# Kernel tuning notes

Hardware: AMD Instinct MI355X
Metric: run time of the kernel (lower is better)

The kernel has to match this reference:

```python
import jax, jax.numpy as jnp
import numpy as np

N = 4096        # number_of_users
IN = 1000       # in_size (items)
H1, H2 = 2048, 1024
EMB = 512
HEADS = 8
OUT = 1000


def setup_inputs() -> dict:
    key = jax.random.key(0)
    ks = iter(jax.random.split(key, 32))
    def lin(i, o):
        return jax.random.normal(next(ks), (i, o), jnp.float32) * (1.0 / np.sqrt(i))
    inp = {"batch": jax.random.normal(next(ks), (N, IN), jnp.float32)}
    for p in ("q", "k", "v"):
        inp[p + "_w1"] = lin(IN, H1); inp[p + "_b1"] = jnp.zeros((H1,), jnp.float32)
        inp[p + "_w2"] = lin(H1, H2); inp[p + "_b2"] = jnp.zeros((H2,), jnp.float32)
        inp[p + "_w3"] = lin(H2, EMB); inp[p + "_b3"] = jnp.zeros((EMB,), jnp.float32)
    inp["wo_w"] = lin(EMB, OUT)
    inp["wo_b"] = jnp.zeros((OUT,), jnp.float32)
    return inp


def _mlp(x, w1, b1, w2, b2, w3, b3):
    h = jax.nn.relu(x @ w1 + b1)
    h = jax.nn.relu(h @ w2 + b2)
    return h @ w3 + b3


def _split_heads(x):
    # [N, EMB] -> [HEADS, N, depth]
    return x.reshape(N, HEADS, EMB // HEADS).transpose(1, 0, 2)


def reference(batch,
              q_w1, q_b1, q_w2, q_b2, q_w3, q_b3,
              k_w1, k_b1, k_w2, k_b2, k_w3, k_b3,
              v_w1, v_b1, v_w2, v_b2, v_w3, v_b3,
              wo_w, wo_b):
    q = _mlp(batch, q_w1, q_b1, q_w2, q_b2, q_w3, q_b3)
    k = _mlp(batch, k_w1, k_b1, k_w2, k_b2, k_w3, k_b3)
    v = _mlp(batch, v_w1, v_b1, v_w2, v_b2, v_w3, v_b3)
    qh = jax.nn.relu(_split_heads(q))
    kh = jax.nn.relu(_split_heads(k))
    vh = _split_heads(v)
    depth = EMB // HEADS
    # ReLU-normalized attention (no softmax): scores / row-sum
    scores = jnp.einsum('hnd,hmd->hnm', qh, kh) / jnp.sqrt(jnp.float32(depth))
    denom = jnp.sum(scores, axis=-1, keepdims=True) + 1e-8
    weights = scores / denom
    att = jnp.einsum('hnm,hmd->hnd', weights, vh)   # [H, N, depth]
    att = att.transpose(1, 0, 2).reshape(N, EMB)
    return att @ wo_w + wo_b
```

## Files before the change

### kernel.cpp

```cpp
#include <hip/hip_runtime.h>
#include <hip/hip_bf16.h>


typedef __attribute__((ext_vector_type(4))) float f32x4;
typedef __attribute__((ext_vector_type(4))) float float4v;
typedef __attribute__((ext_vector_type(8))) short bf16x8;

static constexpr size_t OFF_XB   = 0;
static constexpr size_t OFF_WT1  = OFF_XB   + 8388608;
static constexpr size_t OFF_WT2  = OFF_WT1  + 12582912;
static constexpr size_t OFF_WT3  = OFF_WT2  + 12582912;
static constexpr size_t OFF_MWT  = OFF_WT3  + 3145728;
static constexpr size_t OFF_B1C  = OFF_MWT  + 1048576;
static constexpr size_t OFF_H1   = OFF_B1C  + 24576;
static constexpr size_t OFF_H2   = OFF_H1   + 50331648;
static constexpr size_t OFF_QKV  = OFF_H2   + 25165824;
static constexpr size_t OFF_MP   = OFF_QKV  + 12582912;
static constexpr size_t OFF_MF   = OFF_MP   + 4259840;
static constexpr size_t OFF_QT   = OFF_MF   + 133120;

__device__ __forceinline__ void gload16(const __hip_bfloat16* g, __hip_bfloat16* l) {
  __builtin_amdgcn_global_load_lds(
      (const __attribute__((address_space(1))) void*)g,
      (__attribute__((address_space(3))) void*)l, 16, 0, 0);
}

__device__ __forceinline__ void xcd_map(int gx, int gy, int cm, int cn,
                                        int& zz, int& mt, int& nt) {
  const int gid = (blockIdx.z * gy + blockIdx.y) * gx + blockIdx.x;
  const int xcd = gid & 7;
  const int slot = gid >> 3;
  const int per = cm * cn;
  zz = slot / per;
  const int rem = slot % per;
  const int nxr = gx / cn;
  const int xr = xcd % nxr, yr = xcd / nxr;
  mt = yr * cm + rem % cm;
  nt = xr * cn + rem / cm;
}

__global__ __launch_bounds__(256) void prep(
    const float* __restrict__ w1a, const float* __restrict__ w1b, const float* __restrict__ w1c,
    const float* __restrict__ w2a, const float* __restrict__ w2b, const float* __restrict__ w2c,
    const float* __restrict__ w3a, const float* __restrict__ w3b, const float* __restrict__ w3c,
    const float* __restrict__ batch,
    __hip_bfloat16* __restrict__ WT1, __hip_bfloat16* __restrict__ WT2,
    __hip_bfloat16* __restrict__ WT3, __hip_bfloat16* __restrict__ XB) {
  __shared__ float tile[32][33];
  const int b = blockIdx.x, t = threadIdx.x;
  if (b >= 13824) {
    int idx = (b - 13824) * 256 + t;
    int row = idx >> 8, c4 = (idx & 255) * 4;
    __hip_bfloat16 o[4];
    if (c4 < 1000) {
      float4v v = *reinterpret_cast<const float4v*>(&batch[(size_t)row * 1000 + c4]);
#pragma unroll
      for (int j = 0; j < 4; ++j) o[j] = __float2bfloat16(v[j]);
    } else {
#pragma unroll
      for (int j = 0; j < 4; ++j) o[j] = __float2bfloat16(0.f);
    }
    *reinterpret_cast<ushort4*>(&XB[(size_t)row * 1024 + c4]) =
        *reinterpret_cast<const ushort4*>(o);
    return;
  }
  const float* in; __hip_bfloat16* out; int K, N, Kpad, kb, nb;
  if (b < 6144) {
    int mat = b >> 11, r = b & 2047;
    const float* s[3] = {w1a, w1b, w1c};
    in = s[mat]; out = WT1 + (size_t)mat * 2048 * 1024;
    K = 1000; N = 2048; Kpad = 1024; kb = r & 31; nb = r >> 5;
  } else if (b < 12288) {
    int r = b - 6144; int mat = r >> 11; r &= 2047;
    const float* s[3] = {w2a, w2b, w2c};
    in = s[mat]; out = WT2 + (size_t)mat * 1024 * 2048;
    K = 2048; N = 1024; Kpad = 2048; kb = r & 63; nb = r >> 6;
  } else {
    int r = b - 12288; int mat = r >> 9; r &= 511;
    const float* s[3] = {w3a, w3b, w3c};
    in = s[mat]; out = WT3 + (size_t)mat * 512 * 1024;
    K = 1024; N = 512; Kpad = 1024; kb = r & 31; nb = r >> 5;
  }
  const int tx = t & 31, ty = t >> 5;
  const int kb32 = kb * 32, nb32 = nb * 32;
  for (int i = ty; i < 32; i += 8) {
    int k = kb32 + i, n = nb32 + tx;
    tile[i][tx] = (k < K && n < N) ? in[(size_t)k * N + n] : 0.f;
  }
  __syncthreads();
  for (int i = ty; i < 32; i += 8) {
    int n = nb32 + i, kp = kb32 + tx;
    out[(size_t)n * Kpad + kp] = __float2bfloat16(tile[tx][i]);
  }
}

__global__ __launch_bounds__(256) void gemm_fast(
    const __hip_bfloat16* __restrict__ A, int lda, size_t Az,
    const __hip_bfloat16* __restrict__ B, int ldb, size_t Bz,
    const float* __restrict__ bias0, const float* __restrict__ bias1,
    const float* __restrict__ bias2,
    void* __restrict__ Cout, int ldc, size_t Cz,
    int nlimit, int NT, int epi, int cm, int cn) {
  __shared__ __hip_bfloat16 smA[2][4096];
  __shared__ __hip_bfloat16 smB[2][4096];
  const int t = threadIdx.x;
  int zz, mt, nt;
  xcd_map(gridDim.x, gridDim.y, cm, cn, zz, mt, nt);
  const int m0 = mt * 128, n0 = nt * 128;
  A += (size_t)zz * Az;
  B += (size_t)zz * Bz;

  const int w = t >> 6, l = t & 63;
  const int wm = (w >> 1) * 64, wn = (w & 1) * 64;
  const int fr = l & 15, fq = l >> 4;

  const int r0 = t >> 2;
  const int cg = (t & 3) ^ ((t >> 3) & 3);
  const __hip_bfloat16* gA0 = A + (size_t)(m0 + r0) * lda + cg * 8;
  const __hip_bfloat16* gA1 = gA0 + (size_t)64 * lda;
  const __hip_bfloat16* gB0 = B + (size_t)(n0 + r0) * ldb + cg * 8;
  const __hip_bfloat16* gB1 = gB0 + (size_t)64 * ldb;

  const int soff = (fq ^ ((fr >> 1) & 3)) * 8;
  int offA[4], offB[4];
#pragma unroll
  for (int i = 0; i < 4; ++i) {
    offA[i] = (wm + i * 16 + fr) * 32 + soff;
    offB[i] = (wn + i * 16 + fr) * 32 + soff;
  }

  f32x4 acc[4][4] = {};

  gload16(gA0, &smA[0][w * 512]);
  gload16(gA1, &smA[0][w * 512 + 2048]);
  gload16(gB0, &smB[0][w * 512]);
  gload16(gB1, &smB[0][w * 512 + 2048]);
  asm volatile("s_waitcnt vmcnt(0)" ::: "memory");
  __builtin_amdgcn_s_barrier();

  for (int T = 0; T < NT; ++T) {
    const int cur = T & 1, nxt = cur ^ 1;
    if (T > 0) {
      asm volatile("s_waitcnt vmcnt(0) lgkmcnt(0)" ::: "memory");
      __builtin_amdgcn_sched_barrier(0);
      __builtin_amdgcn_s_barrier();
    }
    bf16x8 af[4], bf[4];
#pragma unroll
    for (int i = 0; i < 4; ++i) {
      af[i] = *reinterpret_cast<const bf16x8*>(&smA[cur][offA[i]]);
      bf[i] = *reinterpret_cast<const bf16x8*>(&smB[cur][offB[i]]);
    }
    if (T + 1 < NT) {
      const size_t ko = (size_t)(T + 1) * 32;
      gload16(gA0 + ko, &smA[nxt][w * 512]);
      gload16(gA1 + ko, &smA[nxt][w * 512 + 2048]);
      gload16(gB0 + ko, &smB[nxt][w * 512]);
      gload16(gB1 + ko, &smB[nxt][w * 512 + 2048]);
    }
    __builtin_amdgcn_s_setprio(1);
#pragma unroll
    for (int i = 0; i < 4; ++i)
#pragma unroll
      for (int j = 0; j < 4; ++j)
        acc[i][j] = __builtin_amdgcn_mfma_f32_16x16x32_bf16(af[i], bf[j], acc[i][j], 0, 0, 0);
    __builtin_amdgcn_s_setprio(0);
  }

  const float* bz = (zz == 0) ? bias0 : ((zz == 1) ? bias1 : bias2);
  const bool dorelu = (epi == 1) || (epi == 4) || (epi == 3 && zz < 2);
  float bv[4];
#pragma unroll
  for (int j = 0; j < 4; ++j) {
    const int col = n0 + wn + j * 16 + fr;
    if (epi == 4) {
      const float* bsel = (col < 2048) ? bias0 : ((col < 4096) ? bias1 : bias2);
      bv[j] = bsel[col & 2047];
    } else if (epi == 2) {
      bv[j] = (col < nlimit) ? bias0[col] : 0.f;
    } else {
      bv[j] = bz[col];
    }
  }
#pragma unroll
  for (int i = 0; i < 4; ++i) {
#pragma unroll
    for (int j = 0; j < 4; ++j) {
      const int col = n0 + wn + j * 16 + fr;
#pragma unroll
      for (int rr = 0; rr < 4; ++rr) {
        const int row = m0 + wm + i * 16 + fq * 4 + rr;
        float v = acc[i][j][rr] + bv[j];
        if (dorelu) v = fmaxf(v, 0.f);
        if (epi == 2) {
          if (col < nlimit)
            ((float*)Cout)[(size_t)row * ldc + col] = v;
        } else {
          ((__hip_bfloat16*)Cout + (size_t)zz * Cz)[(size_t)row * ldc + col] =
              __float2bfloat16(v);
        }
      }
    }
  }
}

__global__ __launch_bounds__(256) void kv_outer(const __hip_bfloat16* __restrict__ QKV, int ld,
                                                float* __restrict__ part) {
  __shared__ __hip_bfloat16 kt[128][64];
  __shared__ __hip_bfloat16 vt[128][64];
  const int t = threadIdx.x;
  const int n0 = blockIdx.x * 128;
  const int h = blockIdx.y;
#pragma unroll
  for (int it = 0; it < 4; ++it) {
    int r = it * 32 + (t >> 3);
    int c = (t & 7) * 8;
    const __hip_bfloat16* kr = &QKV[(size_t)(n0 + r) * ld + 512 + h * 64 + c];
    const __hip_bfloat16* vr = &QKV[(size_t)(n0 + r) * ld + 1024 + h * 64 + c];
    *reinterpret_cast<bf16x8*>(&kt[r][c]) = *reinterpret_cast<const bf16x8*>(kr);
    *reinterpret_cast<bf16x8*>(&vt[r][c]) = *reinterpret_cast<const bf16x8*>(vr);
  }
  __syncthreads();
  const int i = t >> 2, j0 = (t & 3) << 4;
  float acc[16] = {};
  float ks = 0.f;
  for (int r = 0; r < 128; ++r) {
    float kv = __bfloat162float(kt[r][i]);
    ks += kv;
    bf16x8 va = *reinterpret_cast<const bf16x8*>(&vt[r][j0]);
    bf16x8 vb = *reinterpret_cast<const bf16x8*>(&vt[r][j0 + 8]);
#pragma unroll
    for (int jj = 0; jj < 8; ++jj) {
      ushort ua = (ushort)((const short*)&va)[jj];
      ushort ub = (ushort)((const short*)&vb)[jj];
      acc[jj]     += kv * __bfloat162float(*(const __hip_bfloat16*)&ua);
      acc[8 + jj] += kv * __bfloat162float(*(const __hip_bfloat16*)&ub);
    }
  }
  float* dst = part + ((size_t)blockIdx.x * 8 + h) * 4160;
#pragma unroll
  for (int jj = 0; jj < 16; ++jj) dst[i * 64 + j0 + jj] = acc[jj];
  if ((t & 3) == 0) dst[4096 + i] = ks;
}

__global__ void reduce_m(const float* __restrict__ part, float* __restrict__ Mfin) {
  int h = blockIdx.x, t = threadIdx.x;
  for (int idx = t; idx < 4160; idx += 256) {
    float s = 0.f;
    for (int c = 0; c < 32; ++c) s += part[((size_t)c * 8 + h) * 4160 + idx];
    Mfin[(size_t)h * 4160 + idx] = s;
  }
}

__global__ __launch_bounds__(256) void mwq(const float* __restrict__ Mfin,
                                           const float* __restrict__ wo,
                                           __hip_bfloat16* __restrict__ MWT,
                                           const __hip_bfloat16* __restrict__ QKV,
                                           __hip_bfloat16* __restrict__ QT) {
  const int t = threadIdx.x;
  if (blockIdx.x < 32) {
    __shared__ float Ml[64][64];
    const int h = blockIdx.x >> 2;
    const int j = (blockIdx.x & 3) * 256 + t;
    const float* M = Mfin + (size_t)h * 4160;
    for (int e = t; e < 4096; e += 256)
      Ml[e >> 6][e & 63] = M[e];
    __syncthreads();
    float wcol[64];
    const bool valid = (j < 1000);
#pragma unroll
    for (int d = 0; d < 64; ++d)
      wcol[d] = valid ? wo[(size_t)(h * 64 + d) * 1000 + j] : 0.f;
    short ob[64];
#pragma unroll
    for (int i = 0; i < 64; ++i) {
      float a = 0.f;
#pragma unroll
      for (int d = 0; d < 64; ++d) a += Ml[i][d] * wcol[d];
      __hip_bfloat16 bb = __float2bfloat16(a);
      ob[i] = *(const short*)&bb;
    }
    __hip_bfloat16* dst = MWT + (size_t)j * 512 + h * 64;
#pragma unroll
    for (int v = 0; v < 8; ++v)
      *reinterpret_cast<bf16x8*>(dst + v * 8) = *reinterpret_cast<const bf16x8*>(&ob[v * 8]);
  } else {
    const int bid = blockIdx.x - 32;
    const int r = bid * 4 + (t >> 6);
    const int c = (t & 63) * 8;
    const int h = (t & 63) >> 3;
    bf16x8 qv = *reinterpret_cast<const bf16x8*>(&QKV[(size_t)r * 1536 + c]);
    float qf[8];
#pragma unroll
    for (int j = 0; j < 8; ++j) {
      ushort u = (ushort)((const short*)&qv)[j];
      qf[j] = __bfloat162float(*(const __hip_bfloat16*)&u);
    }
    const float* ks = Mfin + (size_t)h * 4160 + 4096 + (c & 63);
    float s = 0.f;
#pragma unroll
    for (int j = 0; j < 8; ++j) s += qf[j] * ks[j];
    s += __shfl_xor(s, 1, 8);
    s += __shfl_xor(s, 2, 8);
    s += __shfl_xor(s, 4, 8);
    const float inv = 0.125f / (s * 0.125f + 1e-8f);
    bf16x8 o;
#pragma unroll
    for (int j = 0; j < 8; ++j) {
      __hip_bfloat16 bb = __float2bfloat16(qf[j] * inv);
      ((short*)&o)[j] = *(const short*)&bb;
    }
    *reinterpret_cast<bf16x8*>(&QT[(size_t)r * 512 + c]) = o;
  }
}

extern "C" void kernel_launch(void* const* d_in, const int* in_sizes, int n_in,
                              void* d_out, int out_size, void* d_ws, size_t ws_size,
                              hipStream_t stream) {
  const float* batch = (const float*)d_in[0];
  const float* w1[3] = {(const float*)d_in[1],  (const float*)d_in[7],  (const float*)d_in[13]};
  const float* b1[3] = {(const float*)d_in[2],  (const float*)d_in[8],  (const float*)d_in[14]};
  const float* w2[3] = {(const float*)d_in[3],  (const float*)d_in[9],  (const float*)d_in[15]};
  const float* b2[3] = {(const float*)d_in[4],  (const float*)d_in[10], (const float*)d_in[16]};
  const float* w3[3] = {(const float*)d_in[5],  (const float*)d_in[11], (const float*)d_in[17]};
  const float* b3[3] = {(const float*)d_in[6],  (const float*)d_in[12], (const float*)d_in[18]};
  const float* wow   = (const float*)d_in[19];
  const float* wob   = (const float*)d_in[20];

  char* ws = (char*)d_ws;
  __hip_bfloat16* XB  = (__hip_bfloat16*)(ws + OFF_XB);
  __hip_bfloat16* WT1 = (__hip_bfloat16*)(ws + OFF_WT1);
  __hip_bfloat16* WT2 = (__hip_bfloat16*)(ws + OFF_WT2);
  __hip_bfloat16* WT3 = (__hip_bfloat16*)(ws + OFF_WT3);
  __hip_bfloat16* MWT = (__hip_bfloat16*)(ws + OFF_MWT);
  __hip_bfloat16* H1  = (__hip_bfloat16*)(ws + OFF_H1);
  __hip_bfloat16* H2  = (__hip_bfloat16*)(ws + OFF_H2);
  __hip_bfloat16* QKV = (__hip_bfloat16*)(ws + OFF_QKV);
  float*          MP  = (float*)(ws + OFF_MP);
  float*          MF  = (float*)(ws + OFF_MF);
  __hip_bfloat16* QT  = (__hip_bfloat16*)(ws + OFF_QT);
  float*          OUT = (float*)d_out;

  prep<<<17920, 256, 0, stream>>>(w1[0], w1[1], w1[2], w2[0], w2[1], w2[2],
                                  w3[0], w3[1], w3[2], batch, WT1, WT2, WT3, XB);

  gemm_fast<<<dim3(48, 32, 1), 256, 0, stream>>>(XB, 1024, 0, WT1, 1024, 0,
                                                 b1[0], b1[1], b1[2], H1, 6144, 0,
                                                 6144, 32, 4, 16, 12);
  gemm_fast<<<dim3(8, 32, 3), 256, 0, stream>>>(H1, 6144, 2048, WT2, 2048,
                                                (size_t)1024 * 2048,
                                                b2[0], b2[1], b2[2], H2, 3072, 1024,
                                                1024, 64, 1, 8, 4);
  gemm_fast<<<dim3(4, 32, 3), 256, 0, stream>>>(H2, 3072, 1024, WT3, 1024,
                                                (size_t)512 * 1024,
                                                b3[0], b3[1], b3[2], QKV, 1536, 512,
                                                512, 32, 3, 8, 2);

  kv_outer<<<dim3(32, 8), 256, 0, stream>>>(QKV, 1536, MP);
  reduce_m<<<8, 256, 0, stream>>>(MP, MF);
  mwq<<<1056, 256, 0, stream>>>(MF, wow, MWT, QKV, QT);

  gemm_fast<<<dim3(8, 32, 1), 256, 0, stream>>>(QT, 512, 0, MWT, 512, 0,
                                                wob, wob, wob, OUT, 1000, 0,
                                                1000, 16, 2, 8, 4);

  (void)in_sizes; (void)n_in; (void)out_size; (void)ws_size;
}
```

Before: 282.3 us.

## Triple-buffer GEMM K-loop and vectorize 64x64 weight transpose in prep

The GEMM main loop moves from double to triple buffering. Tiles are prefetched two steps ahead, and a partial `vmcnt(4)` wait replaces the full vmcnt/lgkmcnt drain before each barrier, so global-to-LDS loads overlap more compute. This uses 50% more LDS per block, which may lower occupancy. Separately, the weight transpose-and-cast in prep now works on 64x64 tiles with float4 global loads and 16-byte bf16 stores, cutting block count and improving memory-access width.

Result: no change. 278.7 us (-1.3%).

```diff
diff --git a/kernel.cpp b/kernel.cpp
--- a/kernel.cpp
+++ b/kernel.cpp
@@ -46,10 +46,9 @@
     const float* __restrict__ batch,
     __hip_bfloat16* __restrict__ WT1, __hip_bfloat16* __restrict__ WT2,
     __hip_bfloat16* __restrict__ WT3, __hip_bfloat16* __restrict__ XB) {
-  __shared__ float tile[32][33];
   const int b = blockIdx.x, t = threadIdx.x;
-  if (b >= 13824) {
-    int idx = (b - 13824) * 256 + t;
+  if (b >= 3456) {
+    int idx = (b - 3456) * 256 + t;
     int row = idx >> 8, c4 = (idx & 255) * 4;
     __hip_bfloat16 o[4];
     if (c4 < 1000) {
@@ -64,34 +63,46 @@
         *reinterpret_cast<const ushort4*>(o);
     return;
   }
+  __shared__ float tl[64][65];
   const float* in; __hip_bfloat16* out; int K, N, Kpad, kb, nb;
-  if (b < 6144) {
-    int mat = b >> 11, r = b & 2047;
+  if (b < 1536) {
+    int mat = b / 512, r = b % 512;
     const float* s[3] = {w1a, w1b, w1c};
     in = s[mat]; out = WT1 + (size_t)mat * 2048 * 1024;
-    K = 1000; N = 2048; Kpad = 1024; kb = r & 31; nb = r >> 5;
-  } else if (b < 12288) {
-    int r = b - 6144; int mat = r >> 11; r &= 2047;
+    K = 1000; N = 2048; Kpad = 1024; kb = r & 15; nb = r >> 4;
+  } else if (b < 3072) {
+    int r = b - 1536; int mat = r / 512; r %= 512;
     const float* s[3] = {w2a, w2b, w2c};
     in = s[mat]; out = WT2 + (size_t)mat * 1024 * 2048;
-    K = 2048; N = 1024; Kpad = 2048; kb = r & 63; nb = r >> 6;
+    K = 2048; N = 1024; Kpad = 2048; kb = r & 31; nb = r >> 5;
   } else {
-    int r = b - 12288; int mat = r >> 9; r &= 511;
+    int r = b - 3072; int mat = r / 128; r %= 128;
     const float* s[3] = {w3a, w3b, w3c};
     in = s[mat]; out = WT3 + (size_t)mat * 512 * 1024;
-    K = 1024; N = 512; Kpad = 1024; kb = r & 31; nb = r >> 5;
-  }
-  const int tx = t & 31, ty = t >> 5;
-  const int kb32 = kb * 32, nb32 = nb * 32;
-  for (int i = ty; i < 32; i += 8) {
-    int k = kb32 + i, n = nb32 + tx;
-    tile[i][tx] = (k < K && n < N) ? in[(size_t)k * N + n] : 0.f;
+    K = 1024; N = 512; Kpad = 1024; kb = r & 15; nb = r >> 4;
+  }
+  const int kb64 = kb * 64, nb64 = nb * 64;
+  const int trow = t >> 4, tc4 = (t & 15) * 4;
+#pragma unroll
+  for (int it = 0; it < 4; ++it) {
+    const int kl = it * 16 + trow;
+    const int k = kb64 + kl;
+    float4v v = {0.f, 0.f, 0.f, 0.f};
+    if (k < K) v = *reinterpret_cast<const float4v*>(&in[(size_t)k * N + nb64 + tc4]);
+    tl[kl][tc4 + 0] = v[0]; tl[kl][tc4 + 1] = v[1];
+    tl[kl][tc4 + 2] = v[2]; tl[kl][tc4 + 3] = v[3];
   }
   __syncthreads();
-  for (int i = ty; i < 32; i += 8) {
-    int n = nb32 + i, kp = kb32 + tx;
-    out[(size_t)n * Kpad + kp] = __float2bfloat16(tile[tx][i]);
-  }
+  const int ln = t >> 2, ks = (t & 3) * 16;
+  short ob[16];
+#pragma unroll
+  for (int u = 0; u < 16; ++u) {
+    __hip_bfloat16 bb = __float2bfloat16(tl[ks + u][ln]);
+    ob[u] = *(const short*)&bb;
+  }
+  __hip_bfloat16* dst = out + (size_t)(nb64 + ln) * Kpad + kb64 + ks;
+  *reinterpret_cast<bf16x8*>(dst) = *reinterpret_cast<const bf16x8*>(&ob[0]);
+  *reinterpret_cast<bf16x8*>(dst + 8) = *reinterpret_cast<const bf16x8*>(&ob[8]);
 }
 
 __global__ __launch_bounds__(256) void gemm_fast(
@@ -101,8 +112,8 @@
     const float* __restrict__ bias2,
     void* __restrict__ Cout, int ldc, size_t Cz,
     int nlimit, int NT, int epi, int cm, int cn) {
-  __shared__ __hip_bfloat16 smA[2][4096];
-  __shared__ __hip_bfloat16 smB[2][4096];
+  __shared__ __hip_bfloat16 smA[3][4096];
+  __shared__ __hip_bfloat16 smB[3][4096];
   const int t = threadIdx.x;
   int zz, mt, nt;
   xcd_map(gridDim.x, gridDim.y, cm, cn, zz, mt, nt);
@@ -131,32 +142,34 @@
 
   f32x4 acc[4][4] = {};
 
-  gload16(gA0, &smA[0][w * 512]);
-  gload16(gA1, &smA[0][w * 512 + 2048]);
-  gload16(gB0, &smB[0][w * 512]);
-  gload16(gB1, &smB[0][w * 512 + 2048]);
-  asm volatile("s_waitcnt vmcnt(0)" ::: "memory");
-  __builtin_amdgcn_s_barrier();
-
+#define STG(BUF, KT) do {                                                      \
+    const size_t ko_ = (size_t)(KT) * 32;                                      \
+    gload16(gA0 + ko_, &smA[BUF][w * 512]);                                    \
+    gload16(gA1 + ko_, &smA[BUF][w * 512 + 2048]);                             \
+    gload16(gB0 + ko_, &smB[BUF][w * 512]);                                    \
+    gload16(gB1 + ko_, &smB[BUF][w * 512 + 2048]);                             \
+  } while (0)
+
+  STG(0, 0);
+  STG(1, 1);
+
+  int cur = 0;
   for (int T = 0; T < NT; ++T) {
-    const int cur = T & 1, nxt = cur ^ 1;
-    if (T > 0) {
-      asm volatile("s_waitcnt vmcnt(0) lgkmcnt(0)" ::: "memory");
-      __builtin_amdgcn_sched_barrier(0);
-      __builtin_amdgcn_s_barrier();
-    }
+    if (T == NT - 1)
+      asm volatile("s_waitcnt vmcnt(0)" ::: "memory");
+    else
+      asm volatile("s_waitcnt vmcnt(4)" ::: "memory");
+    __builtin_amdgcn_s_barrier();
+    __builtin_amdgcn_sched_barrier(0);
     bf16x8 af[4], bf[4];
 #pragma unroll
     for (int i = 0; i < 4; ++i) {
       af[i] = *reinterpret_cast<const bf16x8*>(&smA[cur][offA[i]]);
       bf[i] = *reinterpret_cast<const bf16x8*>(&smB[cur][offB[i]]);
     }
-    if (T + 1 < NT) {
-      const size_t ko = (size_t)(T + 1) * 32;
-      gload16(gA0 + ko, &smA[nxt][w * 512]);
-      gload16(gA1 + ko, &smA[nxt][w * 512 + 2048]);
-      gload16(gB0 + ko, &smB[nxt][w * 512]);
-      gload16(gB1 + ko, &smB[nxt][w * 512 + 2048]);
+    if (T + 2 < NT) {
+      const int nb_ = (cur + 2 >= 3) ? cur - 1 : cur + 2;
+      STG(nb_, T + 2);
     }
     __builtin_amdgcn_s_setprio(1);
 #pragma unroll
@@ -165,7 +178,9 @@
       for (int j = 0; j < 4; ++j)
         acc[i][j] = __builtin_amdgcn_mfma_f32_16x16x32_bf16(af[i], bf[j], acc[i][j], 0, 0, 0);
     __builtin_amdgcn_s_setprio(0);
-  }
+    cur = (cur + 1 >= 3) ? 0 : cur + 1;
+  }
+#undef STG
 
   const float* bz = (zz == 0) ? bias0 : ((zz == 1) ? bias1 : bias2);
   const bool dorelu = (epi == 1) || (epi == 4) || (epi == 3 && zz < 2);
@@ -341,8 +356,8 @@
   __hip_bfloat16* QT  = (__hip_bfloat16*)(ws + OFF_QT);
   float*          OUT = (float*)d_out;
 
-  prep<<<17920, 256, 0, stream>>>(w1[0], w1[1], w1[2], w2[0], w2[1], w2[2],
-                                  w3[0], w3[1], w3[2], batch, WT1, WT2, WT3, XB);
+  prep<<<7552, 256, 0, stream>>>(w1[0], w1[1], w1[2], w2[0], w2[1], w2[2],
+                                 w3[0], w3[1], w3[2], batch, WT1, WT2, WT3, XB);
 
   gemm_fast<<<dim3(48, 32, 1), 256, 0, stream>>>(XB, 1024, 0, WT1, 1024, 0,
                                                  b1[0], b1[1], b1[2], H1, 6144, 0,
```
